# Kernel tuning notes

Hardware: AMD Instinct MI355X
Metric: run time of the kernel (lower is better)

## Reference

```python
import jax, jax.numpy as jnp
import numpy as np

B, N, D = 4, 2048, 1024
DF = 4 * D
EPS = 1e-5


def _layernorm(x, w, b):
    mu = jnp.mean(x, axis=-1, keepdims=True)
    var = jnp.mean(jnp.square(x - mu), axis=-1, keepdims=True)
    return (x - mu) * jax.lax.rsqrt(var + EPS) * w + b


def setup_inputs() -> dict:
    key = jax.random.key(0)
    ks = jax.random.split(key, 8)
    x = jax.random.normal(ks[0], (B, N, D), dtype=jnp.float32)
    # conv filter param (torch init is zeros; use small randn for numeric coverage)
    weights = jax.random.normal(ks[1], (1, 1, N), dtype=jnp.float32) * 0.02
    # registered buffer: sqrt(1/(i+1)) per token, shape (1, N, 1)
    scale = jnp.sqrt(1.0 / (jnp.arange(N, dtype=jnp.float32) + 1.0))[None, :, None]
    ln1_w = jnp.ones((D,), jnp.float32)
    ln1_b = jnp.zeros((D,), jnp.float32)
    W1 = jax.random.normal(ks[2], (DF, D), dtype=jnp.float32) * 0.02
    b1 = jnp.zeros((DF,), jnp.float32)
    W2 = jax.random.normal(ks[3], (D, DF), dtype=jnp.float32) * 0.02
    b2 = jnp.zeros((D,), jnp.float32)
    scalar = jax.random.normal(ks[4], (1,), dtype=jnp.float32) * 0.1
    ln2_w = jnp.ones((D,), jnp.float32)
    ln2_b = jnp.zeros((D,), jnp.float32)
    return dict(x=x, weights=weights, scale=scale, ln1_w=ln1_w, ln1_b=ln1_b,
                W1=W1, b1=b1, W2=W2, b2=b2, scalar=scalar, ln2_w=ln2_w, ln2_b=ln2_b)


def reference(x, weights, scale, ln1_w, ln1_b, W1, b1, W2, b2, scalar, ln2_w, ln2_b):
    n = weights.shape[-1]
    # FFT token-mixing conv: operate over token axis. x: (B,N,D) -> (B,D,N)
    xt = jnp.swapaxes(x, -2, -1)
    # real inputs -> rfft/irfft equals real(ifft(fft*fft)) from the torch code
    prod = jnp.fft.rfft(xt, n=2 * n) * jnp.fft.rfft(weights, n=2 * n)
    conv = jnp.fft.irfft(prod, n=2 * n)[..., :n]  # (B,D,N)
    x1 = jnp.swapaxes(conv, -2, -1)               # (B,N,D)
    x1 = _layernorm(x + x1 * scale, ln1_w, ln1_b)
    # GELU MLP (torch F.gelu default = exact erf gelu)
    h = jax.nn.gelu(jnp.einsum('bnd,fd->bnf', x1, W1) + b1, approximate=False)
    mlp = jnp.einsum('bnf,df->bnd', h, W2) + b2
    x2 = _layernorm(x1 + scalar * mlp, ln2_w, ln2_b)
    return x2
```

## Files before the change

### kernel.cpp

```cpp
#include <hip/hip_runtime.h>
#include <cstdint>

typedef float floatx4 __attribute__((ext_vector_type(4)));
typedef int intx8 __attribute__((ext_vector_type(8)));

__device__ __forceinline__ unsigned short f2b(float f) {
  union { float f; unsigned u; } v; v.f = f;
  return (unsigned short)((v.u + 0x7FFFu + ((v.u >> 16) & 1u)) >> 16);
}
__device__ __forceinline__ float b2f(unsigned short h) {
  union { unsigned u; float f; } v; v.u = ((unsigned)h) << 16;
  return v.f;
}

__device__ __forceinline__ void gload_lds16(const void* g, void* l) {
  __builtin_amdgcn_global_load_lds(
      (const __attribute__((address_space(1))) void*)g,
      (__attribute__((address_space(3))) void*)l, 16, 0, 0);
}


__global__ void cast_f8x64_kernel(const float* __restrict__ in,
                                  int* __restrict__ out) {
  long i = (long)blockIdx.x * 256 + threadIdx.x;
  float4 v = ((const float4*)in)[i];
  int pk = __builtin_amdgcn_cvt_pk_fp8_f32(v.x * 64.0f, v.y * 64.0f, 0, false);
  pk = __builtin_amdgcn_cvt_pk_fp8_f32(v.z * 64.0f, v.w * 64.0f, pk, true);
  out[i] = pk;
}

__global__ void build_T8_kernel(const float* __restrict__ w,
                                int* __restrict__ T8) {
  long i = (long)blockIdx.x * 256 + threadIdx.x;
  int n = (int)(i >> 9);
  int m0 = (int)(i & 511) * 4;
  float v[4];
#pragma unroll
  for (int r = 0; r < 4; ++r) {
    int m = m0 + r;
    v[r] = (m <= n) ? w[n - m] * 64.0f : 0.0f;
  }
  int pk = __builtin_amdgcn_cvt_pk_fp8_f32(v[0], v[1], 0, false);
  pk = __builtin_amdgcn_cvt_pk_fp8_f32(v[2], v[3], pk, true);
  T8[i] = pk;
}

__global__ void transpose_cast_f8_kernel(const float* __restrict__ x,
                                         unsigned char* __restrict__ xT) {
  __shared__ float tile[32][33];
  int b = blockIdx.z;
  int n0 = blockIdx.y * 32;
  int d0 = blockIdx.x * 32;
  int tx = threadIdx.x;
  int ty = threadIdx.y;
  for (int i = ty; i < 32; i += 8)
    tile[i][tx] = x[((long)b * 2048 + n0 + i) * 1024 + d0 + tx];
  __syncthreads();
  float a = tile[ty * 4 + 0][tx];
  float c = tile[ty * 4 + 1][tx];
  float e = tile[ty * 4 + 2][tx];
  float f = tile[ty * 4 + 3][tx];
  int pk = __builtin_amdgcn_cvt_pk_fp8_f32(a, c, 0, false);
  pk = __builtin_amdgcn_cvt_pk_fp8_f32(e, f, pk, true);
  *(int*)(xT + ((long)b * 1024 + d0 + tx) * 2048 + n0 + ty * 4) = pk;
}

template <int EPI, int NT, bool TRI>
__global__ __launch_bounds__(256, 4) void gemm_f8(
    const unsigned char* __restrict__ A, const unsigned char* __restrict__ B,
    int Kstride, int Kloop, long zsA, long zsB, long zsC,
    int rx, int ryb, int gxn, unsigned sclA, unsigned sclB,
    const float* __restrict__ resid, const float* __restrict__ scale,
    const float* __restrict__ bias,
    float* __restrict__ Cf, unsigned short* __restrict__ Cb,
    unsigned char* __restrict__ C8) {
  __shared__ __align__(16) unsigned char As[16 * 1040];
  __shared__ __align__(16) unsigned char Bs[16 * 1040];
  const int tid = threadIdx.x;
  const int wid = tid >> 6;
  const int lane = tid & 63;
  const int quad = lane >> 4;
  const int l16 = lane & 15;
  const int wm = (wid >> 1) * 64;
  const int wn = (wid & 1) * 64;

  const int bid = blockIdx.x;
  const int xcd = bid & 7;
  const int ib = bid >> 3;
  const int ci = ib % rx;
  const int ri = ib / rx;
  long bm, bn;
  if (TRI) {
    bm = (long)(ri == 0 ? xcd : 15 - xcd) * 128;
    bn = (long)ci * 128;
  } else {
    const int gx = xcd % gxn;
    const int gy = xcd / gxn;
    bm = (long)(gy * ryb + ri) * 128;
    bn = (long)(gx * rx + ci) * 128;
  }
  const int bz = blockIdx.z;
  const unsigned char* Ab = A + zsA * bz;
  const unsigned char* Bb = B + zsB * bz;

  floatx4 acc[4][4];
#pragma unroll
  for (int i = 0; i < 4; ++i)
#pragma unroll
    for (int j = 0; j < 4; ++j)
      acc[i][j] = floatx4{0.0f, 0.0f, 0.0f, 0.0f};

  const int srow = tid >> 3;
  const int scol = (tid & 7) * 16;
  const unsigned char* gA[4];
  const unsigned char* gB[4];
  unsigned char* lA[4];
  unsigned char* lB[4];
#pragma unroll
  for (int p = 0; p < 4; ++p) {
    gA[p] = Ab + (bm + p * 32 + srow) * (long)Kstride + scol;
    gB[p] = Bb + (bn + p * 32 + srow) * (long)Kstride + scol;
    lA[p] = As + (p * 4 + wid) * 1040;
    lB[p] = Bs + (p * 4 + wid) * 1040;
  }

  const int kend = TRI ? min(Kloop, (int)bm + 128) : Kloop;
  for (int kk = 0; kk < kend; kk += 128) {
    __syncthreads();
#pragma unroll
    for (int p = 0; p < 4; ++p) {
      gload_lds16(gA[p] + kk, lA[p]);
      gload_lds16(gB[p] + kk, lB[p]);
    }
    __syncthreads();
    intx8 af[4], bfr[4];
#pragma unroll
    for (int i = 0; i < 4; ++i) {
      const int ra = wm + i * 16 + l16;
      const int off = (ra >> 3) * 1040 + (ra & 7) * 128 + quad * 32;
      union { intx8 v; int4 q[2]; } u;
      u.q[0] = *(const int4*)(As + off);
      u.q[1] = *(const int4*)(As + off + 16);
      af[i] = u.v;
    }
#pragma unroll
    for (int j = 0; j < 4; ++j) {
      const int rb = wn + j * 16 + l16;
      const int off = (rb >> 3) * 1040 + (rb & 7) * 128 + quad * 32;
      union { intx8 v; int4 q[2]; } u;
      u.q[0] = *(const int4*)(Bs + off);
      u.q[1] = *(const int4*)(Bs + off + 16);
      bfr[j] = u.v;
    }
#pragma unroll
    for (int i = 0; i < 4; ++i)
#pragma unroll
      for (int j = 0; j < 4; ++j)
        acc[i][j] = __builtin_amdgcn_mfma_scale_f32_16x16x128_f8f6f4(
            af[i], bfr[j], acc[i][j], 0 , 0 ,
            0, sclA, 0, sclB);
  }

#pragma unroll
  for (int i = 0; i < 4; ++i)
#pragma unroll
    for (int j = 0; j < 4; ++j)
#pragma unroll
      for (int r = 0; r < 4; ++r) {
        long row = bm + wm + i * 16 + quad * 4 + r;
        long col = bn + wn + j * 16 + l16;
        long idx = (long)bz * zsC + row * (long)NT + col;
        float v = acc[i][j][r];
        if (EPI == 0) {
          Cb[idx] = f2b(v);
        } else if (EPI == 1) {
          Cf[idx] = resid[idx] + scale[row] * v;
        } else {
          v += bias[col];
          float u = v * (0.7978845608f + 0.0356774081f * v * v);
          float u2 = u * u;
          float t = __fdividef(u * (15.0f + u2), 15.0f + 6.0f * u2);
          t = fminf(fmaxf(t, -1.0f), 1.0f);
          float g = 0.5f * v * (1.0f + t);
          int pk = __builtin_amdgcn_cvt_pk_fp8_f32(g, 0.0f, 0, false);
          C8[idx] = (unsigned char)(pk & 0xFF);
        }
      }
}

template <int EPI, int NT>
__global__ __launch_bounds__(512, 2) void gemm_f8_256(
    const unsigned char* __restrict__ A, const unsigned char* __restrict__ B,
    int Kstride, int Kloop, long zsA, long zsB, long zsC,
    int rx, int ryb, int gxn, unsigned sclA, unsigned sclB,
    const float* __restrict__ bias,
    unsigned short* __restrict__ Cb, unsigned char* __restrict__ C8) {
  __shared__ __align__(16) unsigned char As[2 * 32 * 1040];
  __shared__ __align__(16) unsigned char Bs[2 * 32 * 1040];
  const int tid = threadIdx.x;
  const int wid = tid >> 6;
  const int lane = tid & 63;
  const int quad = lane >> 4;
  const int l16 = lane & 15;
  const int wm = (wid >> 2) * 128;
  const int wn = (wid & 3) * 64;

  const int bid = blockIdx.x;
  const int xcd = bid & 7;
  const int ib = bid >> 3;
  const int ci = ib % rx;
  const int ri = ib / rx;
  const int gx = xcd % gxn;
  const int gy = xcd / gxn;
  const long bm = (long)(gy * ryb + ri) * 256;
  const long bn = (long)(gx * rx + ci) * 256;
  const int bz = blockIdx.z;
  const unsigned char* Ab = A + zsA * bz;
  const unsigned char* Bb = B + zsB * bz;

  floatx4 acc[8][4];
#pragma unroll
  for (int i = 0; i < 8; ++i)
#pragma unroll
    for (int j = 0; j < 4; ++j)
      acc[i][j] = floatx4{0.0f, 0.0f, 0.0f, 0.0f};

  const int srow = wid * 8 + (lane >> 3);
  const int scol = (lane & 7) * 16;
  const unsigned char* gA[4];
  const unsigned char* gB[4];
  unsigned char* lA[4];
  unsigned char* lB[4];
#pragma unroll
  for (int p = 0; p < 4; ++p) {
    gA[p] = Ab + (bm + p * 64 + srow) * (long)Kstride + scol;
    gB[p] = Bb + (bn + p * 64 + srow) * (long)Kstride + scol;
    lA[p] = As + (p * 8 + wid) * 1040;
    lB[p] = Bs + (p * 8 + wid) * 1040;
  }

  int offA[8], offB[4];
#pragma unroll
  for (int i = 0; i < 8; ++i) {
    const int ra = wm + i * 16 + l16;
    offA[i] = (ra >> 3) * 1040 + (ra & 7) * 128 + quad * 32;
  }
#pragma unroll
  for (int j = 0; j < 4; ++j) {
    const int rb = wn + j * 16 + l16;
    offB[j] = (rb >> 3) * 1040 + (rb & 7) * 128 + quad * 32;
  }

#pragma unroll
  for (int p = 0; p < 4; ++p) {
    gload_lds16(gA[p], lA[p]);
    gload_lds16(gB[p], lB[p]);
  }

  int so = 0;
  for (int kk = 0; kk < Kloop; kk += 128) {
    const int kn = kk + 128;
    if (kn < Kloop) {
      const int po = so ^ 33280;
#pragma unroll
      for (int p = 0; p < 4; ++p) {
        gload_lds16(gA[p] + kn, lA[p] + po);
        gload_lds16(gB[p] + kn, lB[p] + po);
      }
      asm volatile("s_waitcnt vmcnt(8)" ::: "memory");
    } else {
      asm volatile("s_waitcnt vmcnt(0)" ::: "memory");
    }
    __builtin_amdgcn_s_barrier();

    intx8 bfr[4];
#pragma unroll
    for (int j = 0; j < 4; ++j) {
      union { intx8 v; int4 q[2]; } u;
      u.q[0] = *(const int4*)(Bs + so + offB[j]);
      u.q[1] = *(const int4*)(Bs + so + offB[j] + 16);
      bfr[j] = u.v;
    }
    __builtin_amdgcn_s_setprio(1);
#pragma unroll
    for (int i = 0; i < 8; ++i) {
      union { intx8 v; int4 q[2]; } u;
      u.q[0] = *(const int4*)(As + so + offA[i]);
      u.q[1] = *(const int4*)(As + so + offA[i] + 16);
      intx8 af = u.v;
#pragma unroll
      for (int j = 0; j < 4; ++j)
        acc[i][j] = __builtin_amdgcn_mfma_scale_f32_16x16x128_f8f6f4(
            af, bfr[j], acc[i][j], 0 , 0 ,
            0, sclA, 0, sclB);
    }
    __builtin_amdgcn_s_setprio(0);
    __builtin_amdgcn_s_barrier();
    so ^= 33280;
  }

#pragma unroll
  for (int i = 0; i < 8; ++i)
#pragma unroll
    for (int j = 0; j < 4; ++j)
#pragma unroll
      for (int r = 0; r < 4; ++r) {
        long row = bm + wm + i * 16 + quad * 4 + r;
        long col = bn + wn + j * 16 + l16;
        long idx = (long)bz * zsC + row * (long)NT + col;
        float v = acc[i][j][r];
        if (EPI == 0) {
          Cb[idx] = f2b(v);
        } else {
          v += bias[col];
          float u = v * (0.7978845608f + 0.0356774081f * v * v);
          float u2 = u * u;
          float t = __fdividef(u * (15.0f + u2), 15.0f + 6.0f * u2);
          t = fminf(fmaxf(t, -1.0f), 1.0f);
          float g = 0.5f * v * (1.0f + t);
          int pk = __builtin_amdgcn_cvt_pk_fp8_f32(g, 0.0f, 0, false);
          C8[idx] = (unsigned char)(pk & 0xFF);
        }
      }
}

__global__ __launch_bounds__(256) void ln_kernel(
    const float* __restrict__ in, const float* __restrict__ w,
    const float* __restrict__ b, unsigned short* __restrict__ outb,
    int* __restrict__ outf8) {
  const long row = blockIdx.x;
  const int tid = threadIdx.x;
  float4 v = ((const float4*)in)[row * 256 + tid];
  float s = v.x + v.y + v.z + v.w;
  float ss = v.x * v.x + v.y * v.y + v.z * v.z + v.w * v.w;
#pragma unroll
  for (int off = 32; off > 0; off >>= 1) {
    s += __shfl_down(s, off);
    ss += __shfl_down(ss, off);
  }
  __shared__ float red[8];
  const int wid = tid >> 6, lane = tid & 63;
  if (lane == 0) { red[wid] = s; red[4 + wid] = ss; }
  __syncthreads();
  s = red[0] + red[1] + red[2] + red[3];
  ss = red[4] + red[5] + red[6] + red[7];
  const float mu = s * (1.0f / 1024.0f);
  const float var = ss * (1.0f / 1024.0f) - mu * mu;
  const float rs = rsqrtf(var + 1e-5f);
  float4 wv = ((const float4*)w)[tid];
  float4 bv = ((const float4*)b)[tid];
  float o0 = (v.x - mu) * rs * wv.x + bv.x;
  float o1 = (v.y - mu) * rs * wv.y + bv.y;
  float o2 = (v.z - mu) * rs * wv.z + bv.z;
  float o3 = (v.w - mu) * rs * wv.w + bv.w;
  ushort4 u{f2b(o0), f2b(o1), f2b(o2), f2b(o3)};
  ((ushort4*)outb)[row * 256 + tid] = u;
  int pk = __builtin_amdgcn_cvt_pk_fp8_f32(o0, o1, 0, false);
  pk = __builtin_amdgcn_cvt_pk_fp8_f32(o2, o3, pk, true);
  outf8[row * 256 + tid] = pk;
}

__global__ __launch_bounds__(256) void ln2_fused_kernel(
    const unsigned short* __restrict__ y0, const unsigned short* __restrict__ y1,
    const unsigned short* __restrict__ x1b, const float* __restrict__ b2,
    const float* __restrict__ scalar_p, const float* __restrict__ w,
    const float* __restrict__ b, float* __restrict__ out) {
  const long row = blockIdx.x;
  const int tid = threadIdx.x;
  ushort4 a4 = ((const ushort4*)y0)[row * 256 + tid];
  ushort4 c4 = ((const ushort4*)y1)[row * 256 + tid];
  ushort4 xr = ((const ushort4*)x1b)[row * 256 + tid];
  float4 bias = ((const float4*)b2)[tid];
  const float scl = scalar_p[0];
  float4 v;
  v.x = b2f(xr.x) + scl * (b2f(a4.x) + b2f(c4.x) + bias.x);
  v.y = b2f(xr.y) + scl * (b2f(a4.y) + b2f(c4.y) + bias.y);
  v.z = b2f(xr.z) + scl * (b2f(a4.z) + b2f(c4.z) + bias.z);
  v.w = b2f(xr.w) + scl * (b2f(a4.w) + b2f(c4.w) + bias.w);
  float s = v.x + v.y + v.z + v.w;
  float ss = v.x * v.x + v.y * v.y + v.z * v.z + v.w * v.w;
#pragma unroll
  for (int off = 32; off > 0; off >>= 1) {
    s += __shfl_down(s, off);
    ss += __shfl_down(ss, off);
  }
  __shared__ float red[8];
  const int wid = tid >> 6, lane = tid & 63;
  if (lane == 0) { red[wid] = s; red[4 + wid] = ss; }
  __syncthreads();
  s = red[0] + red[1] + red[2] + red[3];
  ss = red[4] + red[5] + red[6] + red[7];
  const float mu = s * (1.0f / 1024.0f);
  const float var = ss * (1.0f / 1024.0f) - mu * mu;
  const float rs = rsqrtf(var + 1e-5f);
  float4 wv = ((const float4*)w)[tid];
  float4 bv = ((const float4*)b)[tid];
  float4 o;
  o.x = (v.x - mu) * rs * wv.x + bv.x;
  o.y = (v.y - mu) * rs * wv.y + bv.y;
  o.z = (v.z - mu) * rs * wv.z + bv.z;
  o.w = (v.w - mu) * rs * wv.w + bv.w;
  ((float4*)out)[row * 256 + tid] = o;
}

extern "C" void kernel_launch(void* const* d_in, const int* in_sizes, int n_in,
                              void* d_out, int out_size, void* d_ws, size_t ws_size,
                              hipStream_t stream) {
  const float* x      = (const float*)d_in[0];
  const float* wconv  = (const float*)d_in[1];
  const float* scale  = (const float*)d_in[2];
  const float* ln1w   = (const float*)d_in[3];
  const float* ln1b   = (const float*)d_in[4];
  const float* W1     = (const float*)d_in[5];
  const float* b1     = (const float*)d_in[6];
  const float* W2     = (const float*)d_in[7];
  const float* b2     = (const float*)d_in[8];
  const float* scalar = (const float*)d_in[9];
  const float* ln2w   = (const float*)d_in[10];
  const float* ln2b   = (const float*)d_in[11];
  float* out = (float*)d_out;

  const unsigned SCL_1  = 0x7F7F7F7Fu;
  const unsigned SCL_64 = 0x79797979u;

  char* ws = (char*)d_ws;
  unsigned char* xT8   = (unsigned char*)ws;  ws += (size_t)4 * 1024 * 2048;
  unsigned char* T8    = (unsigned char*)ws;  ws += (size_t)2048 * 2048;
  unsigned char* W1f8  = (unsigned char*)ws;  ws += (size_t)4096 * 1024;
  unsigned char* W2f8  = (unsigned char*)ws;  ws += (size_t)4096 * 1024;
  float* y             = (float*)ws;          ws += (size_t)8192 * 1024 * 4;
  unsigned short* yb   = (unsigned short*)ws; ws += (size_t)2 * 8192 * 1024 * 2;
  unsigned short* x1b  = (unsigned short*)ws; ws += (size_t)8192 * 1024 * 2;
  unsigned char* x1f8  = (unsigned char*)ws;  ws += (size_t)8192 * 1024;
  unsigned char* h8    = (unsigned char*)ws;  ws += (size_t)8192 * 4096;

  cast_f8x64_kernel<<<4096, 256, 0, stream>>>(W1, (int*)W1f8);
  cast_f8x64_kernel<<<4096, 256, 0, stream>>>(W2, (int*)W2f8);
  build_T8_kernel<<<4096, 256, 0, stream>>>(wconv, (int*)T8);
  transpose_cast_f8_kernel<<<dim3(32, 64, 4), dim3(32, 8), 0, stream>>>(x, xT8);

  gemm_f8<1, 1024, true><<<dim3(128, 1, 4), 256, 0, stream>>>(
      T8, xT8, 2048, 2048, 0L, (long)1024 * 2048, (long)2048 * 1024,
      8, 0, 0, SCL_64, SCL_1, x, scale, nullptr, y, nullptr, nullptr);
  ln_kernel<<<8192, 256, 0, stream>>>(y, ln1w, ln1b, x1b, (int*)x1f8);
  gemm_f8_256<2, 4096><<<dim3(512, 1, 1), 512, 0, stream>>>(
      x1f8, W1f8, 1024, 1024, 0L, 0L, 0L,
      8, 8, 2, SCL_1, SCL_64, b1, nullptr, h8);
  gemm_f8_256<0, 1024><<<dim3(128, 1, 2), 512, 0, stream>>>(
      h8, W2f8, 4096, 2048, 2048L, 2048L, (long)8192 * 1024,
      4, 4, 1, SCL_1, SCL_64, nullptr, yb, nullptr);
  ln2_fused_kernel<<<8192, 256, 0, stream>>>(
      yb, yb + (size_t)8192 * 1024, x1b, b2, scalar, ln2w, ln2b, out);
}
```

Before: 301.1 us.

## Swizzle LDS tiles and split FP8 GEMM main loop into interleaved phases

Applies an XOR swizzle to the 16-byte column chunks written by the global-to-LDS loads and to the matching fragment read offsets in both FP8 GEMM kernels, to reduce LDS bank conflicts. The 256-tile kernel's main loop is rewritten into four barrier-separated phases. Each phase loads two A fragments, issues part of the next tile's global loads, and runs eight MFMAs at raised priority, so memory traffic interleaves with compute across waves. The extra barriers and explicit waitcnt placement add synchronisation overhead and depend on the swizzle being consistent between writes and reads.

Measured after the change: 299.5 us. Within noise of the previous version (-0.5%).

```diff
diff --git a/kernel.cpp b/kernel.cpp
--- a/kernel.cpp
+++ b/kernel.cpp
@@ -17,6 +17,20 @@
   __builtin_amdgcn_global_load_lds(
       (const __attribute__((address_space(1))) void*)g,
       (__attribute__((address_space(3))) void*)l, 16, 0, 0);
+}
+
+__device__ __forceinline__ intx8 lds_read32(const unsigned char* p) {
+  union { intx8 v; int4 q[2]; } u;
+  u.q[0] = *(const int4*)p;
+  u.q[1] = *(const int4*)(p + 16);
+  return u.v;
+}
+
+__device__ __forceinline__ int swz_scol(int lane) {
+  const int q = (lane >> 1) & 3;
+  const int r3 = (lane >> 3) & 3;
+  const int sbit = lane & 1;
+  return ((((q ^ r3) << 1) | sbit) << 4);
 }
 
 
@@ -111,7 +125,7 @@
       acc[i][j] = floatx4{0.0f, 0.0f, 0.0f, 0.0f};
 
   const int srow = tid >> 3;
-  const int scol = (tid & 7) * 16;
+  const int scol = swz_scol(lane);
   const unsigned char* gA[4];
   const unsigned char* gB[4];
   unsigned char* lA[4];
@@ -137,28 +151,21 @@
 #pragma unroll
     for (int i = 0; i < 4; ++i) {
       const int ra = wm + i * 16 + l16;
-      const int off = (ra >> 3) * 1040 + (ra & 7) * 128 + quad * 32;
-      union { intx8 v; int4 q[2]; } u;
-      u.q[0] = *(const int4*)(As + off);
-      u.q[1] = *(const int4*)(As + off + 16);
-      af[i] = u.v;
+      const int off = (ra >> 3) * 1040 + (ra & 7) * 128 + ((quad ^ (ra & 3)) << 5);
+      af[i] = lds_read32(As + off);
     }
 #pragma unroll
     for (int j = 0; j < 4; ++j) {
       const int rb = wn + j * 16 + l16;
-      const int off = (rb >> 3) * 1040 + (rb & 7) * 128 + quad * 32;
-      union { intx8 v; int4 q[2]; } u;
-      u.q[0] = *(const int4*)(Bs + off);
-      u.q[1] = *(const int4*)(Bs + off + 16);
-      bfr[j] = u.v;
+      const int off = (rb >> 3) * 1040 + (rb & 7) * 128 + ((quad ^ (rb & 3)) << 5);
+      bfr[j] = lds_read32(Bs + off);
     }
 #pragma unroll
     for (int i = 0; i < 4; ++i)
 #pragma unroll
       for (int j = 0; j < 4; ++j)
         acc[i][j] = __builtin_amdgcn_mfma_scale_f32_16x16x128_f8f6f4(
-            af[i], bfr[j], acc[i][j], 0 , 0 ,
-            0, sclA, 0, sclB);
+            af[i], bfr[j], acc[i][j], 0, 0, 0, sclA, 0, sclB);
   }
 
 #pragma unroll
@@ -226,7 +233,7 @@
       acc[i][j] = floatx4{0.0f, 0.0f, 0.0f, 0.0f};
 
   const int srow = wid * 8 + (lane >> 3);
-  const int scol = (lane & 7) * 16;
+  const int scol = swz_scol(lane);
   const unsigned char* gA[4];
   const unsigned char* gB[4];
   unsigned char* lA[4];
@@ -243,12 +250,12 @@
 #pragma unroll
   for (int i = 0; i < 8; ++i) {
     const int ra = wm + i * 16 + l16;
-    offA[i] = (ra >> 3) * 1040 + (ra & 7) * 128 + quad * 32;
+    offA[i] = (ra >> 3) * 1040 + (ra & 7) * 128 + ((quad ^ (ra & 3)) << 5);
   }
 #pragma unroll
   for (int j = 0; j < 4; ++j) {
     const int rb = wn + j * 16 + l16;
-    offB[j] = (rb >> 3) * 1040 + (rb & 7) * 128 + quad * 32;
+    offB[j] = (rb >> 3) * 1040 + (rb & 7) * 128 + ((quad ^ (rb & 3)) << 5);
   }
 
 #pragma unroll
@@ -256,48 +263,96 @@
     gload_lds16(gA[p], lA[p]);
     gload_lds16(gB[p], lB[p]);
   }
+  asm volatile("s_waitcnt vmcnt(0)" ::: "memory");
+  __builtin_amdgcn_s_barrier();
+
+#define LGKM0() do { asm volatile("s_waitcnt lgkmcnt(0)" ::: "memory"); \
+                     __builtin_amdgcn_sched_barrier(0); } while (0)
 
   int so = 0;
   for (int kk = 0; kk < Kloop; kk += 128) {
     const int kn = kk + 128;
-    if (kn < Kloop) {
-      const int po = so ^ 33280;
-#pragma unroll
-      for (int p = 0; p < 4; ++p) {
-        gload_lds16(gA[p] + kn, lA[p] + po);
-        gload_lds16(gB[p] + kn, lB[p] + po);
-      }
-      asm volatile("s_waitcnt vmcnt(8)" ::: "memory");
-    } else {
-      asm volatile("s_waitcnt vmcnt(0)" ::: "memory");
-    }
-    __builtin_amdgcn_s_barrier();
-
-    intx8 bfr[4];
+    const bool nxt = kn < Kloop;
+    const int po = so ^ 33280;
+    intx8 bfr[4], af0, af1;
+
+#pragma unroll
+    for (int j = 0; j < 4; ++j) bfr[j] = lds_read32(Bs + so + offB[j]);
+    af0 = lds_read32(As + so + offA[0]);
+    af1 = lds_read32(As + so + offA[1]);
+    if (nxt) {
+      gload_lds16(gA[0] + kn, lA[0] + po);
+      gload_lds16(gA[1] + kn, lA[1] + po);
+      gload_lds16(gB[0] + kn, lB[0] + po);
+      gload_lds16(gB[1] + kn, lB[1] + po);
+    }
+    __builtin_amdgcn_s_barrier();
+    LGKM0();
+    __builtin_amdgcn_s_setprio(1);
 #pragma unroll
     for (int j = 0; j < 4; ++j) {
-      union { intx8 v; int4 q[2]; } u;
-      u.q[0] = *(const int4*)(Bs + so + offB[j]);
-      u.q[1] = *(const int4*)(Bs + so + offB[j] + 16);
-      bfr[j] = u.v;
-    }
+      acc[0][j] = __builtin_amdgcn_mfma_scale_f32_16x16x128_f8f6f4(
+          af0, bfr[j], acc[0][j], 0, 0, 0, sclA, 0, sclB);
+      acc[1][j] = __builtin_amdgcn_mfma_scale_f32_16x16x128_f8f6f4(
+          af1, bfr[j], acc[1][j], 0, 0, 0, sclA, 0, sclB);
+    }
+    __builtin_amdgcn_s_setprio(0);
+    __builtin_amdgcn_s_barrier();
+
+    af0 = lds_read32(As + so + offA[2]);
+    af1 = lds_read32(As + so + offA[3]);
+    if (nxt) {
+      gload_lds16(gA[2] + kn, lA[2] + po);
+      gload_lds16(gA[3] + kn, lA[3] + po);
+      gload_lds16(gB[2] + kn, lB[2] + po);
+      gload_lds16(gB[3] + kn, lB[3] + po);
+    }
+    __builtin_amdgcn_s_barrier();
+    LGKM0();
     __builtin_amdgcn_s_setprio(1);
 #pragma unroll
-    for (int i = 0; i < 8; ++i) {
-      union { intx8 v; int4 q[2]; } u;
-      u.q[0] = *(const int4*)(As + so + offA[i]);
-      u.q[1] = *(const int4*)(As + so + offA[i] + 16);
-      intx8 af = u.v;
-#pragma unroll
-      for (int j = 0; j < 4; ++j)
-        acc[i][j] = __builtin_amdgcn_mfma_scale_f32_16x16x128_f8f6f4(
-            af, bfr[j], acc[i][j], 0 , 0 ,
-            0, sclA, 0, sclB);
+    for (int j = 0; j < 4; ++j) {
+      acc[2][j] = __builtin_amdgcn_mfma_scale_f32_16x16x128_f8f6f4(
+          af0, bfr[j], acc[2][j], 0, 0, 0, sclA, 0, sclB);
+      acc[3][j] = __builtin_amdgcn_mfma_scale_f32_16x16x128_f8f6f4(
+          af1, bfr[j], acc[3][j], 0, 0, 0, sclA, 0, sclB);
     }
     __builtin_amdgcn_s_setprio(0);
     __builtin_amdgcn_s_barrier();
-    so ^= 33280;
-  }
+
+    af0 = lds_read32(As + so + offA[4]);
+    af1 = lds_read32(As + so + offA[5]);
+    __builtin_amdgcn_s_barrier();
+    LGKM0();
+    __builtin_amdgcn_s_setprio(1);
+#pragma unroll
+    for (int j = 0; j < 4; ++j) {
+      acc[4][j] = __builtin_amdgcn_mfma_scale_f32_16x16x128_f8f6f4(
+          af0, bfr[j], acc[4][j], 0, 0, 0, sclA, 0, sclB);
+      acc[5][j] = __builtin_amdgcn_mfma_scale_f32_16x16x128_f8f6f4(
+          af1, bfr[j], acc[5][j], 0, 0, 0, sclA, 0, sclB);
+    }
+    __builtin_amdgcn_s_setprio(0);
+    __builtin_amdgcn_s_barrier();
+
+    af0 = lds_read32(As + so + offA[6]);
+    af1 = lds_read32(As + so + offA[7]);
+    __builtin_amdgcn_s_barrier();
+    LGKM0();
+    __builtin_amdgcn_s_setprio(1);
+#pragma unroll
+    for (int j = 0; j < 4; ++j) {
+      acc[6][j] = __builtin_amdgcn_mfma_scale_f32_16x16x128_f8f6f4(
+          af0, bfr[j], acc[6][j], 0, 0, 0, sclA, 0, sclB);
+      acc[7][j] = __builtin_amdgcn_mfma_scale_f32_16x16x128_f8f6f4(
+          af1, bfr[j], acc[7][j], 0, 0, 0, sclA, 0, sclB);
+    }
+    __builtin_amdgcn_s_setprio(0);
+    if (nxt) asm volatile("s_waitcnt vmcnt(0)" ::: "memory");
+    __builtin_amdgcn_s_barrier();
+    so = po;
+  }
+#undef LGKM0
 
 #pragma unroll
   for (int i = 0; i < 8; ++i)
```
